# Performance work log

Hardware: AMD Instinct MI355X
Metric: run time of the kernel (lower is better)

## Reference

```python
import jax, jax.numpy as jnp
import numpy as np

# db4 decomposition filters (as in get_wavelet_filters('db4'))
_H0 = jnp.array([0.0322231, -0.01260397, -0.09921954, 0.2978578,
                 0.80373875, 0.49761867, -0.02963553, -0.07576571], dtype=jnp.float32)
_H1 = jnp.array([0.07576571, -0.02963553, -0.49761867, 0.80373875,
                 -0.2978578, -0.09921954, 0.01260397, 0.0322231], dtype=jnp.float32)
LEVEL = 2
IN_CH, OUT_CH, MODES = 64, 64, 32


def subband_conv2d(x, k2d, stride):
    # depthwise (grouped) conv: same 2D filter applied per channel, NHWC
    C = x.shape[-1]
    k = jnp.tile(k2d[:, :, None, None], (1, 1, 1, C)).astype(x.dtype)  # HWIO, I=1
    return jax.lax.conv_general_dilated(
        x, k, (stride, stride), 'SAME',
        dimension_numbers=('NHWC', 'HWIO', 'NHWC'), feature_group_count=C)


def upsample2d(t):
    B, H, W, C = t.shape
    return jnp.zeros((B, 2 * H, 2 * W, C), t.dtype).at[:, ::2, ::2, :].set(t)


def setup_inputs() -> dict:
    key = jax.random.key(0)
    kx, k1, k2, k3, k4 = jax.random.split(key, 5)
    scale = 1.0 / (IN_CH * OUT_CH)
    wshape = (IN_CH, OUT_CH, MODES, MODES)
    return {
        'x': jax.random.normal(kx, (32, 128, 128, IN_CH), dtype=jnp.float32),
        'weights1': scale * jax.random.uniform(k1, wshape, dtype=jnp.float32),
        'weights2': scale * jax.random.uniform(k2, wshape, dtype=jnp.float32),
        'weights3': scale * jax.random.uniform(k3, wshape, dtype=jnp.float32),
        'weights4': scale * jax.random.uniform(k4, wshape, dtype=jnp.float32),
    }


def reference(x, weights1, weights2, weights3, weights4):
    # H=W=128 == size and divisible by 2**LEVEL: pad branch and effective_level
    # adjustment in the original are no-ops.
    h0, h1 = _H0, _H1
    g0, g1 = h0[::-1], h1[::-1]  # reconstruction filters

    # ---- multi-level 2D DWT (depthwise strided convs per subband) ----
    approx = x
    details = []
    for _ in range(LEVEL):
        lh = subband_conv2d(approx, jnp.outer(h0, h1), 2)
        hl = subband_conv2d(approx, jnp.outer(h1, h0), 2)
        hh = subband_conv2d(approx, jnp.outer(h1, h1), 2)
        approx = subband_conv2d(approx, jnp.outer(h0, h0), 2)
        details.append((lh, hl, hh))

    # ---- per-pixel channel mixing on final LL and last-level details ----
    ah, aw = approx.shape[1], approx.shape[2]
    out_ft = jnp.einsum('bhwi,iohw->bhwo', approx, weights1[:, :, :ah, :aw])
    last_lh, last_hl, last_hh = details[-1]
    dh, dw = last_lh.shape[1], last_lh.shape[2]
    out_lh = jnp.einsum('bhwi,iohw->bhwo', last_lh, weights2[:, :, :dh, :dw])
    out_hl = jnp.einsum('bhwi,iohw->bhwo', last_hl, weights3[:, :, :dh, :dw])
    out_hh = jnp.einsum('bhwi,iohw->bhwo', last_hh, weights4[:, :, :dh, :dw])

    # ---- IDWT reconstruction ----
    # Deepest level: all four subbands contribute. Earlier levels: details are
    # zeroed in the original, and conv(zeros)=0, so only the LL path remains.
    res = (subband_conv2d(upsample2d(out_ft), jnp.outer(g0, g0), 1)
           + subband_conv2d(upsample2d(out_lh), jnp.outer(g0, g1), 1)
           + subband_conv2d(upsample2d(out_hl), jnp.outer(g1, g0), 1)
           + subband_conv2d(upsample2d(out_hh), jnp.outer(g1, g1), 1))
    for _ in range(LEVEL - 1):
        res = subband_conv2d(upsample2d(res), jnp.outer(g0, g0), 1)
    return res
```

## Files before the change

kernel.cpp:

```cpp
#include <hip/hip_runtime.h>


__constant__ float c_h0[8] = {0.0322231f, -0.01260397f, -0.09921954f, 0.2978578f,
                              0.80373875f, 0.49761867f, -0.02963553f, -0.07576571f};
__constant__ float c_h1[8] = {0.07576571f, -0.02963553f, -0.49761867f, 0.80373875f,
                              -0.2978578f, -0.09921954f, 0.01260397f, 0.0322231f};
__constant__ float c_g0[8] = {-0.07576571f, -0.02963553f, 0.49761867f, 0.80373875f,
                              0.2978578f, -0.09921954f, -0.01260397f, 0.0322231f};
__constant__ float c_g1[8] = {0.0322231f, 0.01260397f, -0.09921954f, -0.2978578f,
                              0.80373875f, -0.49761867f, -0.02963553f, 0.07576571f};

__device__ __forceinline__ float4 f4z() { return make_float4(0.f, 0.f, 0.f, 0.f); }
__device__ __forceinline__ float4 f4fma(float4 a, float w, float4 v) {
  a.x = fmaf(w, v.x, a.x); a.y = fmaf(w, v.y, a.y);
  a.z = fmaf(w, v.z, a.z); a.w = fmaf(w, v.w, a.w);
  return a;
}

__global__ __launch_bounds__(256) void k_dwt1(const float* __restrict__ x,
                                              float* __restrict__ ll1) {
  int t = threadIdx.x;
  int c4 = t & 15;
  int owl = t >> 4;
  int bid = blockIdx.x;
  int owb = bid & 3;
  int ohc = (bid >> 2) & 3;
  int b   = bid >> 4;
  int ow  = owb * 16 + owl;
  int oh0 = ohc * 16;
  const float* xb = x + ((size_t)b << 20) + (c4 << 2);
  int iwbase = 2 * ow - 3;

  auto hrow = [&](int ih) -> float4 {
    float4 r = f4z();
    if ((unsigned)ih >= 128u) return r;
    const float* row = xb + ih * 8192;
    float4 v[8];
#pragma unroll
    for (int j = 0; j < 8; ++j) {
      int iw = iwbase + j;
      int iwc = min(max(iw, 0), 127);
      v[j] = *(const float4*)(row + (iwc << 6));
    }
#pragma unroll
    for (int j = 0; j < 8; ++j) {
      int iw = iwbase + j;
      float w = ((unsigned)iw < 128u) ? c_h0[j] : 0.f;
      r = f4fma(r, w, v[j]);
    }
    return r;
  };

  float4 ring[8];
  int ihb = 2 * oh0 - 3;
#pragma unroll
  for (int k = 0; k < 6; ++k) ring[k] = hrow(ihb + k);
  float* outp = ll1 + ((((size_t)b * 64 + oh0) * 64 + ow) << 6) + (c4 << 2);
#pragma unroll
  for (int oo = 0; oo < 16; ++oo) {
    ring[6] = hrow(ihb + 6);
    ring[7] = hrow(ihb + 7);
    float4 a = f4z();
#pragma unroll
    for (int i = 0; i < 8; ++i) a = f4fma(a, c_h0[i], ring[i]);
    *(float4*)(outp + oo * 4096) = a;
#pragma unroll
    for (int k = 0; k < 6; ++k) ring[k] = ring[k + 2];
    ihb += 2;
  }
}

__global__ __launch_bounds__(256) void k_dwt2(const float* __restrict__ ll1,
                                              float* __restrict__ subs) {
  int t = threadIdx.x;
  int c4 = t & 15;
  int owl = t >> 4;
  int bid = blockIdx.x;
  int owb = bid & 1;
  int ohc = (bid >> 1) & 3;
  int b   = bid >> 3;
  int ow  = owb * 16 + owl;
  int oh0 = ohc * 8;
  const float* sb = ll1 + ((size_t)b << 18) + (c4 << 2);
  int iwbase = 2 * ow - 3;

  auto hrow2 = [&](int ih, float4& rl, float4& rh) {
    rl = f4z(); rh = f4z();
    if ((unsigned)ih >= 64u) return;
    const float* row = sb + ih * 4096;
    float4 v[8];
#pragma unroll
    for (int j = 0; j < 8; ++j) {
      int iw = iwbase + j;
      int iwc = min(max(iw, 0), 63);
      v[j] = *(const float4*)(row + (iwc << 6));
    }
#pragma unroll
    for (int j = 0; j < 8; ++j) {
      int iw = iwbase + j;
      bool ok = (unsigned)iw < 64u;
      float wl = ok ? c_h0[j] : 0.f;
      float wh = ok ? c_h1[j] : 0.f;
      rl = f4fma(rl, wl, v[j]);
      rh = f4fma(rh, wh, v[j]);
    }
  };

  float4 Rl[8], Rh[8];
  int ihb = 2 * oh0 - 3;
#pragma unroll
  for (int k = 0; k < 6; ++k) hrow2(ihb + k, Rl[k], Rh[k]);
  float* outp = subs + ((((size_t)b * 32 + oh0) * 32 + ow) << 6) + (c4 << 2);
#pragma unroll
  for (int oo = 0; oo < 8; ++oo) {
    hrow2(ihb + 6, Rl[6], Rh[6]);
    hrow2(ihb + 7, Rl[7], Rh[7]);
    float4 a_ll = f4z(), a_lh = f4z(), a_hl = f4z(), a_hh = f4z();
#pragma unroll
    for (int i = 0; i < 8; ++i) {
      a_ll = f4fma(a_ll, c_h0[i], Rl[i]);
      a_lh = f4fma(a_lh, c_h0[i], Rh[i]);
      a_hl = f4fma(a_hl, c_h1[i], Rl[i]);
      a_hh = f4fma(a_hh, c_h1[i], Rh[i]);
    }
    float* o = outp + oo * 2048;
    *(float4*)(o)           = a_ll;
    *(float4*)(o + 2097152) = a_lh;
    *(float4*)(o + 4194304) = a_hl;
    *(float4*)(o + 6291456) = a_hh;
#pragma unroll
    for (int k = 0; k < 6; ++k) { Rl[k] = Rl[k + 2]; Rh[k] = Rh[k + 2]; }
    ihb += 2;
  }
}

__global__ __launch_bounds__(256) void k_transpose(const float* __restrict__ w1,
                                                   const float* __restrict__ w2,
                                                   const float* __restrict__ w3,
                                                   const float* __restrict__ w4,
                                                   float* __restrict__ wt) {
  __shared__ float tile[32][33];
  int s = blockIdx.z;
  const float* w = (s == 0) ? w1 : (s == 1) ? w2 : (s == 2) ? w3 : w4;
  int hw0 = blockIdx.x * 32;
  int io0 = blockIdx.y * 32;
  int tx = threadIdx.x & 31;
  int ty = threadIdx.x >> 5;
#pragma unroll
  for (int k = 0; k < 4; ++k) {
    int r = ty + k * 8;
    tile[r][tx] = w[(io0 + r) * 1024 + hw0 + tx];
  }
  __syncthreads();
  float* o = wt + (size_t)s * 4194304;
#pragma unroll
  for (int k = 0; k < 4; ++k) {
    int r = ty + k * 8;
    o[(hw0 + r) * 4096 + io0 + tx] = tile[tx][r];
  }
}

__global__ __launch_bounds__(256) void k_einsum(const float* __restrict__ subs,
                                               const float* __restrict__ w1,
                                               const float* __restrict__ w2,
                                               const float* __restrict__ w3,
                                               const float* __restrict__ w4,
                                               const float* __restrict__ wt,
                                               float* __restrict__ eout,
                                               int use_wt) {
  __shared__ float sW[4096];
  __shared__ float sA[2048];
  int p = blockIdx.x;
  int s = blockIdx.y;
  int t = threadIdx.x;
  const float* A = subs + (size_t)s * 2097152;
  if (use_wt) {
    const float* Wp = wt + (size_t)s * 4194304 + (size_t)p * 4096;
#pragma unroll
    for (int k = 0; k < 16; ++k) sW[t + 256 * k] = Wp[t + 256 * k];
  } else {
    const float* Ws = (s == 0) ? w1 : (s == 1) ? w2 : (s == 2) ? w3 : w4;
#pragma unroll
    for (int k = 0; k < 16; ++k) {
      int e = t + 256 * k;
      sW[e] = Ws[e * 1024 + p];
    }
  }
#pragma unroll
  for (int k = 0; k < 8; ++k) {
    int e = t + 256 * k;
    sA[e] = A[(e >> 6) * 65536 + (p << 6) + (e & 63)];
  }
  __syncthreads();
  int o  = t & 63;
  int bg = t >> 6;
  float acc[8] = {0.f, 0.f, 0.f, 0.f, 0.f, 0.f, 0.f, 0.f};
  for (int i = 0; i < 64; ++i) {
    float wv = sW[(i << 6) + o];
#pragma unroll
    for (int k = 0; k < 8; ++k) acc[k] += sA[((bg * 8 + k) << 6) + i] * wv;
  }
  float* Oo = eout + (size_t)s * 2097152 + (p << 6) + o;
#pragma unroll
  for (int k = 0; k < 8; ++k) Oo[(bg * 8 + k) * 65536] = acc[k];
}

__global__ __launch_bounds__(256) void k_invres(const float* __restrict__ eout,
                                                float* __restrict__ res) {
  int t = threadIdx.x;
  int c4 = t & 15;
  int ql = t >> 4;
  int bid = blockIdx.x;
  int qb = bid & 1;
  int rc = (bid >> 1) & 3;
  int b  = bid >> 3;
  int q  = qb * 16 + ql;
  int r0 = rc * 8;

  float4 Ae[4], Ao[4], Be[4], Bo[4];
  auto loadrow = [&](int m, float4& ae, float4& ao, float4& be, float4& bo) {
    ae = f4z(); ao = f4z(); be = f4z(); bo = f4z();
    if ((unsigned)m >= 32u) return;
    const float* base = eout + ((((size_t)b * 32 + m) * 32) << 6) + (c4 << 2);
    float4 vf[4], vl[4], vh[4], vv[4];
#pragma unroll
    for (int dn = -1; dn <= 2; ++dn) {
      int n = q + dn;
      int nc = min(max(n, 0), 31);
      const float* p = base + (nc << 6);
      vf[dn + 1] = *(const float4*)(p);
      vl[dn + 1] = *(const float4*)(p + 2097152);
      vh[dn + 1] = *(const float4*)(p + 4194304);
      vv[dn + 1] = *(const float4*)(p + 6291456);
    }
#pragma unroll
    for (int dn = -1; dn <= 2; ++dn) {
      int n = q + dn;
      bool ok = (unsigned)n < 32u;
      float g0e = ok ? c_g0[2 * dn + 3] : 0.f, g1e = ok ? c_g1[2 * dn + 3] : 0.f;
      float g0o = ok ? c_g0[2 * dn + 2] : 0.f, g1o = ok ? c_g1[2 * dn + 2] : 0.f;
      ae = f4fma(ae, g0e, vf[dn + 1]); ae = f4fma(ae, g1e, vl[dn + 1]);
      ao = f4fma(ao, g0o, vf[dn + 1]); ao = f4fma(ao, g1o, vl[dn + 1]);
      be = f4fma(be, g0e, vh[dn + 1]); be = f4fma(be, g1e, vv[dn + 1]);
      bo = f4fma(bo, g0o, vh[dn + 1]); bo = f4fma(bo, g1o, vv[dn + 1]);
    }
  };

#pragma unroll
  for (int k = 0; k < 3; ++k) loadrow(r0 - 1 + k, Ae[k], Ao[k], Be[k], Bo[k]);
#pragma unroll
  for (int rr = 0; rr < 8; ++rr) {
    int r = r0 + rr;
    loadrow(r + 2, Ae[3], Ao[3], Be[3], Bo[3]);
    float4 ee = f4z(), eo = f4z(), oe = f4z(), oo = f4z();
#pragma unroll
    for (int dm = 0; dm < 4; ++dm) {
      float gye = c_g0[2 * dm + 1], hye = c_g1[2 * dm + 1];
      float gyo = c_g0[2 * dm],     hyo = c_g1[2 * dm];
      ee = f4fma(ee, gye, Ae[dm]); ee = f4fma(ee, hye, Be[dm]);
      eo = f4fma(eo, gye, Ao[dm]); eo = f4fma(eo, hye, Bo[dm]);
      oe = f4fma(oe, gyo, Ae[dm]); oe = f4fma(oe, hyo, Be[dm]);
      oo = f4fma(oo, gyo, Ao[dm]); oo = f4fma(oo, hyo, Bo[dm]);
    }
    int y = 2 * r, xx = 2 * q;
    float* ob = res + (((size_t)(b * 64 + y)) * 64 + xx) * 64 + (c4 << 2);
    *(float4*)(ob)                = ee;
    *(float4*)(ob + 64)           = eo;
    *(float4*)(ob + 4096)         = oe;
    *(float4*)(ob + 4096 + 64)    = oo;
#pragma unroll
    for (int k = 0; k < 3; ++k) {
      Ae[k] = Ae[k + 1]; Ao[k] = Ao[k + 1]; Be[k] = Be[k + 1]; Bo[k] = Bo[k + 1];
    }
  }
}

__global__ __launch_bounds__(256) void k_final(const float* __restrict__ res,
                                               float* __restrict__ out) {
  int t = threadIdx.x;
  int c4 = t & 15;
  int ql = t >> 4;
  int bid = blockIdx.x;
  int qb = bid & 3;
  int rc = (bid >> 2) & 3;
  int b  = bid >> 4;
  int q  = qb * 16 + ql;
  int r0 = rc * 16;

  float4 R0[4], R1[4];
  auto loadrow = [&](int m, float4& row0, float4& row1) {
    row0 = f4z(); row1 = f4z();
    if ((unsigned)m >= 64u) return;
    const float* base = res + (((size_t)(b * 64 + m)) * 64) * 64 + (c4 << 2);
    float4 v[4];
#pragma unroll
    for (int dn = -1; dn <= 2; ++dn) {
      int n = q + dn;
      int nc = min(max(n, 0), 63);
      v[dn + 1] = *(const float4*)(base + (nc << 6));
    }
#pragma unroll
    for (int dn = -1; dn <= 2; ++dn) {
      int n = q + dn;
      bool ok = (unsigned)n < 64u;
      float we = ok ? c_g0[2 * dn + 3] : 0.f;
      float wo = ok ? c_g0[2 * dn + 2] : 0.f;
      row0 = f4fma(row0, we, v[dn + 1]);
      row1 = f4fma(row1, wo, v[dn + 1]);
    }
  };

#pragma unroll
  for (int k = 0; k < 3; ++k) loadrow(r0 - 1 + k, R0[k], R1[k]);
#pragma unroll
  for (int rr = 0; rr < 16; ++rr) {
    int r = r0 + rr;
    loadrow(r + 2, R0[3], R1[3]);
    float4 aee = f4z(), aeo = f4z(), aoe = f4z(), aoo = f4z();
#pragma unroll
    for (int dm = 0; dm < 4; ++dm) {
      float gye = c_g0[2 * dm + 1];
      float gyo = c_g0[2 * dm];
      aee = f4fma(aee, gye, R0[dm]);
      aeo = f4fma(aeo, gye, R1[dm]);
      aoe = f4fma(aoe, gyo, R0[dm]);
      aoo = f4fma(aoo, gyo, R1[dm]);
    }
    int y = 2 * r, xx = 2 * q;
    float* ob = out + (((size_t)(b * 128 + y)) * 128 + xx) * 64 + (c4 << 2);
    *(float4*)(ob)                 = aee;
    *(float4*)(ob + 64)            = aeo;
    *(float4*)(ob + 8192)          = aoe;
    *(float4*)(ob + 8192 + 64)     = aoo;
#pragma unroll
    for (int k = 0; k < 3; ++k) { R0[k] = R0[k + 1]; R1[k] = R1[k + 1]; }
  }
}

extern "C" void kernel_launch(void* const* d_in, const int* in_sizes, int n_in,
                              void* d_out, int out_size, void* d_ws, size_t ws_size,
                              hipStream_t stream) {
  (void)in_sizes; (void)n_in; (void)out_size;
  const float* x  = (const float*)d_in[0];
  const float* w1 = (const float*)d_in[1];
  const float* w2 = (const float*)d_in[2];
  const float* w3 = (const float*)d_in[3];
  const float* w4 = (const float*)d_in[4];
  float* out = (float*)d_out;
  float* ws  = (float*)d_ws;

  float* ll1  = ws;
  float* subs = ws + 8388608;
  float* eout = ws + 16777216;
  float* res  = ws;
  float* wt   = ws + 25165824;
  int use_wt = (ws_size >= (size_t)41943040 * 4) ? 1 : 0;

  k_dwt1<<<512, 256, 0, stream>>>(x, ll1);
  if (use_wt) k_transpose<<<dim3(32, 128, 4), 256, 0, stream>>>(w1, w2, w3, w4, wt);
  k_dwt2<<<256, 256, 0, stream>>>(ll1, subs);
  k_einsum<<<dim3(1024, 4), 256, 0, stream>>>(subs, w1, w2, w3, w4, wt, eout, use_wt);
  k_invres<<<256, 256, 0, stream>>>(eout, res);
  k_final<<<512, 256, 0, stream>>>(res, out);
}
```

Baseline: 383.1 us.

## Stage input rows in shared memory for DWT kernels and double block count

```diff
diff --git a/kernel.cpp b/kernel.cpp
--- a/kernel.cpp
+++ b/kernel.cpp
@@ -19,34 +19,43 @@
 
 __global__ __launch_bounds__(256) void k_dwt1(const float* __restrict__ x,
                                               float* __restrict__ ll1) {
+  __shared__ float4 sRow[2][40 * 17];
   int t = threadIdx.x;
   int c4 = t & 15;
   int owl = t >> 4;
   int bid = blockIdx.x;
   int owb = bid & 3;
-  int ohc = (bid >> 2) & 3;
-  int b   = bid >> 4;
-  int ow  = owb * 16 + owl;
-  int oh0 = ohc * 16;
-  const float* xb = x + ((size_t)b << 20) + (c4 << 2);
-  int iwbase = 2 * ow - 3;
-
-  auto hrow = [&](int ih) -> float4 {
+  int ohc = (bid >> 2) & 7;
+  int b   = bid >> 5;
+  int ow0 = owb * 16;
+  int ow  = ow0 + owl;
+  int oh0 = ohc * 8;
+  int iw_start = 2 * ow0 - 3;
+  const float* xb = x + ((size_t)b << 20);
+
+  auto stage2 = [&](int ih0) {
+#pragma unroll
+    for (int base = 0; base < 80; base += 16) {
+      int item = base + owl;
+      int rw   = item >= 40 ? 1 : 0;
+      int iw_s = item - rw * 40;
+      int ihc  = min(max(ih0 + rw, 0), 127);
+      int iwc  = min(max(iw_start + iw_s, 0), 127);
+      sRow[rw][iw_s * 17 + c4] =
+          *(const float4*)(xb + (size_t)ihc * 8192 + (iwc << 6) + (c4 << 2));
+    }
+  };
+
+  auto hrowL = [&](int rw, int ih) -> float4 {
     float4 r = f4z();
     if ((unsigned)ih >= 128u) return r;
-    const float* row = xb + ih * 8192;
-    float4 v[8];
 #pragma unroll
     for (int j = 0; j < 8; ++j) {
-      int iw = iwbase + j;
+      int iw  = 2 * ow - 3 + j;
       int iwc = min(max(iw, 0), 127);
-      v[j] = *(const float4*)(row + (iwc << 6));
-    }
-#pragma unroll
-    for (int j = 0; j < 8; ++j) {
-      int iw = iwbase + j;
+      int iw_s = iwc - iw_start;
       float w = ((unsigned)iw < 128u) ? c_h0[j] : 0.f;
-      r = f4fma(r, w, v[j]);
+      r = f4fma(r, w, sRow[rw][iw_s * 17 + c4]);
     }
     return r;
   };
@@ -54,16 +63,25 @@
   float4 ring[8];
   int ihb = 2 * oh0 - 3;
 #pragma unroll
-  for (int k = 0; k < 6; ++k) ring[k] = hrow(ihb + k);
+  for (int pk = 0; pk < 3; ++pk) {
+    stage2(ihb + 2 * pk);
+    __syncthreads();
+    ring[2 * pk]     = hrowL(0, ihb + 2 * pk);
+    ring[2 * pk + 1] = hrowL(1, ihb + 2 * pk + 1);
+    __syncthreads();
+  }
   float* outp = ll1 + ((((size_t)b * 64 + oh0) * 64 + ow) << 6) + (c4 << 2);
 #pragma unroll
-  for (int oo = 0; oo < 16; ++oo) {
-    ring[6] = hrow(ihb + 6);
-    ring[7] = hrow(ihb + 7);
+  for (int oo = 0; oo < 8; ++oo) {
+    stage2(ihb + 6);
+    __syncthreads();
+    ring[6] = hrowL(0, ihb + 6);
+    ring[7] = hrowL(1, ihb + 7);
     float4 a = f4z();
 #pragma unroll
     for (int i = 0; i < 8; ++i) a = f4fma(a, c_h0[i], ring[i]);
     *(float4*)(outp + oo * 4096) = a;
+    __syncthreads();
 #pragma unroll
     for (int k = 0; k < 6; ++k) ring[k] = ring[k + 2];
     ihb += 2;
@@ -72,49 +90,67 @@
 
 __global__ __launch_bounds__(256) void k_dwt2(const float* __restrict__ ll1,
                                               float* __restrict__ subs) {
+  __shared__ float4 sRow[2][40 * 17];
   int t = threadIdx.x;
   int c4 = t & 15;
   int owl = t >> 4;
   int bid = blockIdx.x;
   int owb = bid & 1;
-  int ohc = (bid >> 1) & 3;
-  int b   = bid >> 3;
-  int ow  = owb * 16 + owl;
-  int oh0 = ohc * 8;
-  const float* sb = ll1 + ((size_t)b << 18) + (c4 << 2);
-  int iwbase = 2 * ow - 3;
-
-  auto hrow2 = [&](int ih, float4& rl, float4& rh) {
+  int ohc = (bid >> 1) & 7;
+  int b   = bid >> 4;
+  int ow0 = owb * 16;
+  int ow  = ow0 + owl;
+  int oh0 = ohc * 4;
+  int iw_start = 2 * ow0 - 3;
+  const float* lb = ll1 + ((size_t)b << 18);
+
+  auto stage2 = [&](int ih0) {
+#pragma unroll
+    for (int base = 0; base < 80; base += 16) {
+      int item = base + owl;
+      int rw   = item >= 40 ? 1 : 0;
+      int iw_s = item - rw * 40;
+      int ihc  = min(max(ih0 + rw, 0), 63);
+      int iwc  = min(max(iw_start + iw_s, 0), 63);
+      sRow[rw][iw_s * 17 + c4] =
+          *(const float4*)(lb + (size_t)ihc * 4096 + (iwc << 6) + (c4 << 2));
+    }
+  };
+
+  auto hrow2L = [&](int rw, int ih, float4& rl, float4& rh) {
     rl = f4z(); rh = f4z();
     if ((unsigned)ih >= 64u) return;
-    const float* row = sb + ih * 4096;
-    float4 v[8];
 #pragma unroll
     for (int j = 0; j < 8; ++j) {
-      int iw = iwbase + j;
+      int iw  = 2 * ow - 3 + j;
       int iwc = min(max(iw, 0), 63);
-      v[j] = *(const float4*)(row + (iwc << 6));
-    }
-#pragma unroll
-    for (int j = 0; j < 8; ++j) {
-      int iw = iwbase + j;
+      int iw_s = iwc - iw_start;
       bool ok = (unsigned)iw < 64u;
       float wl = ok ? c_h0[j] : 0.f;
       float wh = ok ? c_h1[j] : 0.f;
-      rl = f4fma(rl, wl, v[j]);
-      rh = f4fma(rh, wh, v[j]);
+      float4 v = sRow[rw][iw_s * 17 + c4];
+      rl = f4fma(rl, wl, v);
+      rh = f4fma(rh, wh, v);
     }
   };
 
   float4 Rl[8], Rh[8];
   int ihb = 2 * oh0 - 3;
 #pragma unroll
-  for (int k = 0; k < 6; ++k) hrow2(ihb + k, Rl[k], Rh[k]);
+  for (int pk = 0; pk < 3; ++pk) {
+    stage2(ihb + 2 * pk);
+    __syncthreads();
+    hrow2L(0, ihb + 2 * pk,     Rl[2 * pk],     Rh[2 * pk]);
+    hrow2L(1, ihb + 2 * pk + 1, Rl[2 * pk + 1], Rh[2 * pk + 1]);
+    __syncthreads();
+  }
   float* outp = subs + ((((size_t)b * 32 + oh0) * 32 + ow) << 6) + (c4 << 2);
 #pragma unroll
-  for (int oo = 0; oo < 8; ++oo) {
-    hrow2(ihb + 6, Rl[6], Rh[6]);
-    hrow2(ihb + 7, Rl[7], Rh[7]);
+  for (int oo = 0; oo < 4; ++oo) {
+    stage2(ihb + 6);
+    __syncthreads();
+    hrow2L(0, ihb + 6, Rl[6], Rh[6]);
+    hrow2L(1, ihb + 7, Rl[7], Rh[7]);
     float4 a_ll = f4z(), a_lh = f4z(), a_hl = f4z(), a_hh = f4z();
 #pragma unroll
     for (int i = 0; i < 8; ++i) {
@@ -128,6 +164,7 @@
     *(float4*)(o + 2097152) = a_lh;
     *(float4*)(o + 4194304) = a_hl;
     *(float4*)(o + 6291456) = a_hh;
+    __syncthreads();
 #pragma unroll
     for (int k = 0; k < 6; ++k) { Rl[k] = Rl[k + 2]; Rh[k] = Rh[k + 2]; }
     ihb += 2;
@@ -356,9 +393,9 @@
   float* wt   = ws + 25165824;
   int use_wt = (ws_size >= (size_t)41943040 * 4) ? 1 : 0;
 
-  k_dwt1<<<512, 256, 0, stream>>>(x, ll1);
+  k_dwt1<<<1024, 256, 0, stream>>>(x, ll1);
   if (use_wt) k_transpose<<<dim3(32, 128, 4), 256, 0, stream>>>(w1, w2, w3, w4, wt);
-  k_dwt2<<<256, 256, 0, stream>>>(ll1, subs);
+  k_dwt2<<<512, 256, 0, stream>>>(ll1, subs);
   k_einsum<<<dim3(1024, 4), 256, 0, stream>>>(subs, w1, w2, w3, w4, wt, eout, use_wt);
   k_invres<<<256, 256, 0, stream>>>(eout, res);
   k_final<<<512, 256, 0, stream>>>(res, out);
```

Result: no change. 385.8 us (+0.7%).
